# Optimization experiments

Measured on AMD Instinct MI355X. Metric: run time of the kernel, lower is better.

Reference implementation:

```python
import jax, jax.numpy as jnp
import numpy as np

N, E, B = 8192, 131072, 256
F_ATOM, D, H, HD, L, FC, BINS = 92, 256, 8, 32, 6, 512, 256
VMIN, VMAX = 0.0, 8.0


def layer_norm(x, g, b, eps=1e-5):
    mu = jnp.mean(x, axis=-1, keepdims=True)
    var = jnp.var(x, axis=-1, keepdims=True)
    return (x - mu) * jax.lax.rsqrt(var + eps) * g + b


def silu(x):
    return x * jax.nn.sigmoid(x)


def setup_inputs() -> dict:
    key = jax.random.key(0)
    ks = iter(jax.random.split(key, 80))

    def lin(fan_in, shape):
        return jax.random.normal(next(ks), shape, jnp.float32) / np.sqrt(fan_in)

    inp = {
        'x': jax.random.normal(next(ks), (N, F_ATOM), jnp.float32),
        'edge_attr': jax.random.normal(next(ks), (E, 3), jnp.float32) * 2.0,
        'edge_index': jax.random.randint(next(ks), (2, E), 0, N, dtype=jnp.int32),
        'batch': jnp.sort(jax.random.randint(next(ks), (N,), 0, B, dtype=jnp.int32)),
        # atom_embedding: Linear(92,256) -> LN -> SiLU -> Linear(256,256)
        'aw1': lin(F_ATOM, (F_ATOM, D)), 'ab1': jnp.zeros((D,)),
        'ag1': jnp.ones((D,)), 'abt1': jnp.zeros((D,)),
        'aw2': lin(D, (D, D)), 'ab2': jnp.zeros((D,)),
        # rbf MLP: Linear(256,256) LN SiLU Linear LN SiLU Linear
        'rw1': lin(BINS, (BINS, D)), 'rb1': jnp.zeros((D,)),
        'rg1': jnp.ones((D,)), 'rbt1': jnp.zeros((D,)),
        'rw2': lin(D, (D, D)), 'rb2': jnp.zeros((D,)),
        'rg2': jnp.ones((D,)), 'rbt2': jnp.zeros((D,)),
        'rw3': lin(D, (D, D)), 'rb3': jnp.zeros((D,)),
        # L stacked PrdnetConv (edge-conditioned multi-head graph attention)
        'Wq': lin(D, (L, D, D)), 'bq': jnp.zeros((L, D)),
        'Wk': lin(D, (L, D, D)), 'bk': jnp.zeros((L, D)),
        'Wv': lin(D, (L, D, D)), 'bv': jnp.zeros((L, D)),
        'We': lin(D, (L, D, D)), 'be': jnp.zeros((L, D)),
        'Wo': lin(D, (L, D, D)), 'bo': jnp.zeros((L, D)),
        'lng': jnp.ones((L, D)), 'lnb': jnp.zeros((L, D)),
        # FC head: Linear(256,512) then fc_out Linear(512,1)
        'fw1': lin(D, (D, FC)), 'fb1': jnp.zeros((FC,)),
        'fow': lin(FC, (FC, 1)), 'fob': jnp.zeros((1,)),
    }
    return inp


def _forward(x, edge_attr, edge_index, batch, aw1, ab1, ag1, abt1, aw2, ab2,
             rw1, rb1, rg1, rbt1, rw2, rb2, rg2, rbt2, rw3, rb3,
             Wq, bq, Wk, bk, Wv, bv, We, be, Wo, bo, lng, lnb,
             fw1, fb1, fow, fob):
    # atom embedding (dropout = identity at inference)
    node = silu(layer_norm(x @ aw1 + ab1, ag1, abt1)) @ aw2 + ab2  # [N, D]

    # RBF expansion of edge lengths, then edge MLP
    d = jnp.linalg.norm(edge_attr, axis=1)  # [E]
    centers = jnp.linspace(VMIN, VMAX, BINS)
    gamma = 1.0 / (centers[1] - centers[0]) ** 2
    rbf = jnp.exp(-gamma * (d[:, None] - centers[None, :]) ** 2)  # [E, BINS]
    e = silu(layer_norm(rbf @ rw1 + rb1, rg1, rbt1))
    e = silu(layer_norm(e @ rw2 + rb2, rg2, rbt2))
    e = e @ rw3 + rb3  # [E, D]

    src, dst = edge_index[0], edge_index[1]
    inv_sqrt = 1.0 / np.sqrt(HD)
    for l in range(L):
        res = node
        q = (node @ Wq[l] + bq[l]).reshape(N, H, HD)
        k = (node @ Wk[l] + bk[l]).reshape(N, H, HD)
        v = (node @ Wv[l] + bv[l]).reshape(N, H, HD)
        ee = (e @ We[l] + be[l]).reshape(E, H, HD)
        kj = k[src] + ee  # edge-conditioned keys [E, H, HD]
        vj = v[src] + ee  # edge-conditioned values
        score = jnp.sum(q[dst] * kj, axis=-1) * inv_sqrt  # [E, H]
        smax = jax.ops.segment_max(score, dst, num_segments=N)  # [N, H]
        ex = jnp.exp(score - smax[dst])
        den = jax.ops.segment_sum(ex, dst, num_segments=N)
        alpha = ex / (den[dst] + 1e-16)  # neighborhood softmax [E, H]
        msg = jax.ops.segment_sum(alpha[:, :, None] * vj, dst, num_segments=N)
        out = msg.reshape(N, D) @ Wo[l] + bo[l]
        out = layer_norm(out, lng[l], lnb[l])
        node = out + res  # residual

    # scatter-mean graph pooling
    sums = jax.ops.segment_sum(node, batch, num_segments=B)  # [B, D]
    cnt = jax.ops.segment_sum(jnp.ones((N,), node.dtype), batch, num_segments=B)
    feats = sums / jnp.clip(cnt, 1.0)[:, None]

    feats = feats @ fw1 + fb1  # single fc layer: no act (i == len-1 in source)
    return feats @ fow + fob  # [B, 1], identity link


def reference(x, edge_attr, edge_index, batch, aw1, ab1, ag1, abt1, aw2, ab2,
              rw1, rb1, rg1, rbt1, rw2, rb2, rg2, rbt2, rw3, rb3,
              Wq, bq, Wk, bk, Wv, bv, We, be, Wo, bo, lng, lnb,
              fw1, fb1, fow, fob):
    return _forward(x, edge_attr, edge_index, batch, aw1, ab1, ag1, abt1, aw2,
                    ab2, rw1, rb1, rg1, rbt1, rw2, rb2, rg2, rbt2, rw3, rb3,
                    Wq, bq, Wk, bk, Wv, bv, We, be, Wo, bo, lng, lnb,
                    fw1, fb1, fow, fob)
```

## Files before the change

kernel.cpp:

```cpp
#include <hip/hip_runtime.h>
#include <hip/hip_bf16.h>
#include <cstddef>

#define NN    8192
#define EE    131072
#define BB    256
#define F_AT  92
#define DD    256
#define HH    8
#define HDIM  32
#define LL    6
#define FCD   512

typedef __hip_bfloat16 bf16;
typedef __attribute__((ext_vector_type(8))) __bf16 bf16x8;
typedef __attribute__((ext_vector_type(4))) float f32x4;

__device__ __forceinline__ float to_f(float x) { return x; }
__device__ __forceinline__ float to_f(bf16 x) { return __bfloat162float(x); }
__device__ __forceinline__ float bfu(unsigned short u) {
    return __uint_as_float(((unsigned)u) << 16);
}
__device__ __forceinline__ unsigned short bfbits(float x) {
    bf16 h = __float2bfloat16(x);
    return *(unsigned short*)&h;
}
__device__ __forceinline__ void store_v(float* p, float v) { *p = v; }
__device__ __forceinline__ void store_v(bf16* p, float v) { *p = __float2bfloat16(v); }

__device__ __forceinline__ float4 load4(const float* p) { return *(const float4*)p; }
__device__ __forceinline__ float4 load4(const bf16* p) {
    const ushort4 r = *(const ushort4*)p;
    return make_float4(bfu(r.x), bfu(r.y), bfu(r.z), bfu(r.w));
}

__device__ __forceinline__ void store_f4(float* p, const float4& f) {
    *(float4*)p = f;
}
__device__ __forceinline__ void store_f4(bf16* p, const float4& f) {
    ushort4 u = {bfbits(f.x), bfbits(f.y), bfbits(f.z), bfbits(f.w)};
    *(ushort4*)p = u;
}

__device__ __forceinline__ bf16x8 ld8(const bf16* p) { return *(const bf16x8*)p; }
__device__ __forceinline__ bf16x8 ld8(const float* p) {
    const float4 f0 = *(const float4*)p;
    const float4 f1 = *(const float4*)(p + 4);
    bf16x8 r;
    r[0] = (__bf16)f0.x; r[1] = (__bf16)f0.y; r[2] = (__bf16)f0.z; r[3] = (__bf16)f0.w;
    r[4] = (__bf16)f1.x; r[5] = (__bf16)f1.y; r[6] = (__bf16)f1.z; r[7] = (__bf16)f1.w;
    return r;
}

__device__ __forceinline__ void async_copy16(const void* g, void* l) {
    __builtin_amdgcn_global_load_lds(
        (const __attribute__((address_space(1))) unsigned int*)g,
        (__attribute__((address_space(3))) unsigned int*)l, 16, 0, 0);
}

__global__ __launch_bounds__(256) void transpose_weights(
    const float* __restrict__ rw1, const float* __restrict__ rw2,
    const float* __restrict__ rw3, const float* __restrict__ aw2,
    const float* __restrict__ Wq, const float* __restrict__ Wk,
    const float* __restrict__ Wv, const float* __restrict__ We,
    const float* __restrict__ Wo, __bf16* __restrict__ out)
{
    __shared__ float tile[64][65];
    const int midx = blockIdx.y;
    const float* src;
    int fam = 0, s = 0;
    if (midx == 0) src = rw1;
    else if (midx == 1) src = rw2;
    else if (midx == 2) src = rw3;
    else if (midx == 3) src = aw2;
    else {
        fam = (midx - 4) / 5; s = (midx - 4) % 5;
        const float* bases[5] = {Wq, Wk, Wv, We, Wo};
        src = bases[s] + (size_t)fam * 65536;
    }
    const bool isqkv = (midx >= 4) && (s < 3);
    __bf16* dstb = isqkv ? (out + (size_t)(4 + 5 * fam) * 65536)
                         : (out + (size_t)midx * 65536);
    const int k0 = (blockIdx.x >> 2) * 64;
    const int n0 = (blockIdx.x & 3) * 64;
    const int c = threadIdx.x & 63;
    const int r0 = threadIdx.x >> 6;
#pragma unroll
    for (int p = 0; p < 16; ++p) {
        const int r = r0 + p * 4;
        tile[r][c] = src[(size_t)(k0 + r) * 256 + n0 + c];
    }
    __syncthreads();
#pragma unroll
    for (int p = 0; p < 16; ++p) {
        const int n = r0 + p * 4;
        const int gr = n0 + n;
        int row = gr;
        if (isqkv) {
            if (s == 1)      row = 256 + ((gr >> 2) << 3) + (gr & 3);
            else if (s == 2) row = 256 + ((gr >> 2) << 3) + 4 + (gr & 3);
        }
        dstb[(size_t)row * 256 + k0 + c] = (__bf16)tile[c][n];
    }
}

__global__ __launch_bounds__(256) void pack_qkv_bias(
    const float* __restrict__ bq, const float* __restrict__ bk,
    const float* __restrict__ bv, float* __restrict__ out)
{
    const int i = blockIdx.x * 256 + threadIdx.x;
    if (i >= LL * 768) return;
    const int l = i / 768, r = i % 768;
    float val; int pos;
    if (r < 256)      { val = bq[l * 256 + r];        pos = r; }
    else if (r < 512) { const int c = r - 256; val = bk[l * 256 + c];
                        pos = 256 + ((c >> 2) << 3) + (c & 3); }
    else              { const int c = r - 512; val = bv[l * 256 + c];
                        pos = 256 + ((c >> 2) << 3) + 4 + (c & 3); }
    out[l * 768 + pos] = val;
}

__global__ __launch_bounds__(256) void combine_w3e(
    const float* __restrict__ rw3, const float* __restrict__ We,
    __bf16* __restrict__ Wt_out)
{
    __shared__ float As[16][65];
    __shared__ float Ws[16][65];
    const int l = blockIdx.z;
    const float* W = We + (size_t)l * 65536;
    __bf16* dst = Wt_out + (size_t)l * 65536;
    const int m0 = blockIdx.x * 64;
    const int n0 = blockIdx.y * 64;
    const int tid = threadIdx.x;
    const int tx = tid & 15, ty = tid >> 4;
    float acc[4][4] = {};

    for (int k0 = 0; k0 < 256; k0 += 16) {
        {
            const int ar = tid >> 2;
            const int ac = (tid & 3) * 4;
#pragma unroll
            for (int j = 0; j < 4; ++j)
                As[ac + j][ar] = rw3[(size_t)(m0 + ar) * 256 + k0 + ac + j];
        }
        {
            const int wr = tid >> 4;
            const int wc = (tid & 15) * 4;
#pragma unroll
            for (int j = 0; j < 4; ++j)
                Ws[wr][wc + j] = W[(size_t)(k0 + wr) * 256 + n0 + wc + j];
        }
        __syncthreads();
#pragma unroll
        for (int kk = 0; kk < 16; ++kk) {
            float a[4], b[4];
#pragma unroll
            for (int i = 0; i < 4; ++i) a[i] = As[kk][ty * 4 + i];
#pragma unroll
            for (int j = 0; j < 4; ++j) b[j] = Ws[kk][tx * 4 + j];
#pragma unroll
            for (int i = 0; i < 4; ++i)
#pragma unroll
                for (int j = 0; j < 4; ++j) acc[i][j] += a[i] * b[j];
        }
        __syncthreads();
    }
#pragma unroll
    for (int i = 0; i < 4; ++i) {
        const int gk = m0 + ty * 4 + i;
#pragma unroll
        for (int j = 0; j < 4; ++j) {
            const int gn = n0 + tx * 4 + j;
            dst[(size_t)gn * 256 + gk] = (__bf16)acc[i][j];
        }
    }
}

__global__ __launch_bounds__(256) void combine_bias(
    const float* __restrict__ rb3, const float* __restrict__ We,
    const float* __restrict__ be, float* __restrict__ out)
{
    const int l = blockIdx.x;
    const int n = threadIdx.x;
    const float* W = We + (size_t)l * 65536;
    float s = be[l * 256 + n];
    for (int m = 0; m < 256; ++m) s += rb3[m] * W[m * 256 + n];
    out[l * 256 + n] = s;
}

__global__ __launch_bounds__(256) void mfma_gemm_ln(
    const bf16* __restrict__ A, const __bf16* __restrict__ Wt,
    const float* __restrict__ bias, const float* __restrict__ g,
    const float* __restrict__ b, bf16* __restrict__ C, int do_silu)
{
    __shared__ __align__(16) __bf16 As[64 * 64];
    __shared__ __align__(16) __bf16 Bs[256 * 64];
    const int tid = threadIdx.x;
    const int m0 = blockIdx.x * 64;
    const int wave = tid >> 6, lane = tid & 63;
    const int lm = lane & 15, lq = lane >> 4;
    const int lrow = lane >> 3;
    const int lcolsw = ((lane & 7) ^ lrow) * 8;

    f32x4 acc[16] = {};

    for (int k0 = 0; k0 < 256; k0 += 64) {
#pragma unroll
        for (int p = 0; p < 2; ++p) {
            const int rbase = wave * 16 + p * 8;
            async_copy16(A + (size_t)(m0 + rbase + lrow) * 256 + k0 + lcolsw,
                         As + rbase * 64);
        }
#pragma unroll
        for (int p = 0; p < 8; ++p) {
            const int rbase = wave * 64 + p * 8;
            async_copy16(Wt + (size_t)(rbase + lrow) * 256 + k0 + lcolsw,
                         Bs + rbase * 64);
        }
        __syncthreads();
#pragma unroll
        for (int ks = 0; ks < 2; ++ks) {
            const int sw = ((ks * 4 + lq) ^ (lm & 7)) * 8;
            const bf16x8 a = *(const bf16x8*)(As + (wave * 16 + lm) * 64 + sw);
#pragma unroll
            for (int j = 0; j < 16; ++j) {
                const bf16x8 bf = *(const bf16x8*)(Bs + (j * 16 + lm) * 64 + sw);
                acc[j] = __builtin_amdgcn_mfma_f32_16x16x32_bf16(a, bf, acc[j], 0, 0, 0);
            }
        }
        __syncthreads();
    }

    float gg[16], bb[16];
#pragma unroll
    for (int j = 0; j < 16; ++j) {
        const float bv = bias[j * 16 + lm];
        gg[j] = g[j * 16 + lm];
        bb[j] = b[j * 16 + lm];
#pragma unroll
        for (int r = 0; r < 4; ++r) acc[j][r] += bv;
    }

#pragma unroll
    for (int r = 0; r < 4; ++r) {
        float s = 0.f, q = 0.f;
#pragma unroll
        for (int j = 0; j < 16; ++j) { const float v = acc[j][r]; s += v; q += v * v; }
#pragma unroll
        for (int msk = 1; msk < 16; msk <<= 1) {
            s += __shfl_xor(s, msk);
            q += __shfl_xor(q, msk);
        }
        const float mean = s * (1.f / 256.f);
        const float var = q * (1.f / 256.f) - mean * mean;
        const float rs = rsqrtf(var + 1e-5f);
        __bf16* erow = Bs + (wave * 16 + lq * 4 + r) * 256;
#pragma unroll
        for (int j = 0; j < 16; ++j) {
            float v = (acc[j][r] - mean) * rs * gg[j] + bb[j];
            if (do_silu) v = v / (1.f + __expf(-v));
            erow[j * 16 + lm] = (__bf16)v;
        }
    }
    __syncthreads();
    {
        __bf16* cbase = (__bf16*)C + (size_t)m0 * 256;
#pragma unroll
        for (int p = 0; p < 8; ++p) {
            const int ofs = (tid + p * 256) * 8;
            *(bf16x8*)(cbase + ofs) = *(const bf16x8*)(Bs + ofs);
        }
    }
}

__global__ __launch_bounds__(256) void mfma_gemm_ln_rbf(
    const float* __restrict__ dcsr, const __bf16* __restrict__ Wt,
    const float* __restrict__ bias, const float* __restrict__ g,
    const float* __restrict__ b, bf16* __restrict__ C)
{
    __shared__ __align__(16) __bf16 As[64 * 64];
    __shared__ __align__(16) __bf16 Bs[256 * 64];
    const int tid = threadIdx.x;
    const int m0 = blockIdx.x * 64;
    const int wave = tid >> 6, lane = tid & 63;
    const int lm = lane & 15, lq = lane >> 4;
    const int lrow = lane >> 3;
    const int lcolsw = ((lane & 7) ^ lrow) * 8;

    const float step = 8.0f / 255.0f;
    const float gamma = 1.0f / (step * step);

    float dv[2];
#pragma unroll
    for (int p = 0; p < 2; ++p)
        dv[p] = dcsr[m0 + wave * 16 + p * 8 + lrow];

    f32x4 acc[16] = {};

    for (int k0 = 0; k0 < 256; k0 += 64) {
#pragma unroll
        for (int p = 0; p < 2; ++p) {
            const int r = wave * 16 + p * 8 + lrow;
            __bf16* dst8 = As + r * 64 + (lane & 7) * 8;
            const int cbase = k0 + lcolsw;
#pragma unroll
            for (int j = 0; j < 8; ++j) {
                const float t = dv[p] - (float)(cbase + j) * step;
                dst8[j] = (__bf16)__expf(-gamma * t * t);
            }
        }
#pragma unroll
        for (int p = 0; p < 8; ++p) {
            const int rbase = wave * 64 + p * 8;
            async_copy16(Wt + (size_t)(rbase + lrow) * 256 + k0 + lcolsw,
                         Bs + rbase * 64);
        }
        __syncthreads();
#pragma unroll
        for (int ks = 0; ks < 2; ++ks) {
            const int sw = ((ks * 4 + lq) ^ (lm & 7)) * 8;
            const bf16x8 a = *(const bf16x8*)(As + (wave * 16 + lm) * 64 + sw);
#pragma unroll
            for (int j = 0; j < 16; ++j) {
                const bf16x8 bf = *(const bf16x8*)(Bs + (j * 16 + lm) * 64 + sw);
                acc[j] = __builtin_amdgcn_mfma_f32_16x16x32_bf16(a, bf, acc[j], 0, 0, 0);
            }
        }
        __syncthreads();
    }

    float gg[16], bb[16];
#pragma unroll
    for (int j = 0; j < 16; ++j) {
        const float bv = bias[j * 16 + lm];
        gg[j] = g[j * 16 + lm];
        bb[j] = b[j * 16 + lm];
#pragma unroll
        for (int r = 0; r < 4; ++r) acc[j][r] += bv;
    }

#pragma unroll
    for (int r = 0; r < 4; ++r) {
        float s = 0.f, q = 0.f;
#pragma unroll
        for (int j = 0; j < 16; ++j) { const float v = acc[j][r]; s += v; q += v * v; }
#pragma unroll
        for (int msk = 1; msk < 16; msk <<= 1) {
            s += __shfl_xor(s, msk);
            q += __shfl_xor(q, msk);
        }
        const float mean = s * (1.f / 256.f);
        const float var = q * (1.f / 256.f) - mean * mean;
        const float rs = rsqrtf(var + 1e-5f);
        __bf16* erow = Bs + (wave * 16 + lq * 4 + r) * 256;
#pragma unroll
        for (int j = 0; j < 16; ++j) {
            float v = (acc[j][r] - mean) * rs * gg[j] + bb[j];
            v = v / (1.f + __expf(-v));
            erow[j * 16 + lm] = (__bf16)v;
        }
    }
    __syncthreads();
    {
        __bf16* cbase = (__bf16*)C + (size_t)m0 * 256;
#pragma unroll
        for (int p = 0; p < 8; ++p) {
            const int ofs = (tid + p * 256) * 8;
            *(bf16x8*)(cbase + ofs) = *(const bf16x8*)(Bs + ofs);
        }
    }
}

__global__ __launch_bounds__(256) void mfma_gemm_ln_res(
    const float* __restrict__ A, const __bf16* __restrict__ Wt,
    const float* __restrict__ bias, const float* __restrict__ g,
    const float* __restrict__ b, float* __restrict__ node)
{
    __shared__ __align__(16) __bf16 As[64 * 72];
    __shared__ __align__(16) __bf16 Bs[256 * 64];
    const int tid = threadIdx.x;
    const int m0 = blockIdx.x * 64;
    const int wave = tid >> 6, lane = tid & 63;
    const int lm = lane & 15, lq = lane >> 4;
    const int lrow = lane >> 3;
    const int lcolsw = ((lane & 7) ^ lrow) * 8;

    f32x4 acc[16] = {};
    const int srow = tid >> 3;
    const int scol = (tid & 7) * 8;

    for (int k0 = 0; k0 < 256; k0 += 64) {
#pragma unroll
        for (int p = 0; p < 2; ++p) {
            const int r = srow + 32 * p;
            *(bf16x8*)(As + r * 72 + scol) = ld8(A + (size_t)(m0 + r) * 256 + k0 + scol);
        }
#pragma unroll
        for (int p = 0; p < 8; ++p) {
            const int rbase = wave * 64 + p * 8;
            async_copy16(Wt + (size_t)(rbase + lrow) * 256 + k0 + lcolsw,
                         Bs + rbase * 64);
        }
        __syncthreads();
#pragma unroll
        for (int ks = 0; ks < 2; ++ks) {
            const int sw = ((ks * 4 + lq) ^ (lm & 7)) * 8;
            const bf16x8 a = *(const bf16x8*)(As + (wave * 16 + lm) * 72 + ks * 32 + lq * 8);
#pragma unroll
            for (int j = 0; j < 16; ++j) {
                const bf16x8 bf = *(const bf16x8*)(Bs + (j * 16 + lm) * 64 + sw);
                acc[j] = __builtin_amdgcn_mfma_f32_16x16x32_bf16(a, bf, acc[j], 0, 0, 0);
            }
        }
        __syncthreads();
    }

    float gg[16], bb[16];
#pragma unroll
    for (int j = 0; j < 16; ++j) {
        const float bv = bias[j * 16 + lm];
        gg[j] = g[j * 16 + lm];
        bb[j] = b[j * 16 + lm];
#pragma unroll
        for (int r = 0; r < 4; ++r) acc[j][r] += bv;
    }

#pragma unroll
    for (int r = 0; r < 4; ++r) {
        float s = 0.f, q = 0.f;
#pragma unroll
        for (int j = 0; j < 16; ++j) { const float v = acc[j][r]; s += v; q += v * v; }
#pragma unroll
        for (int msk = 1; msk < 16; msk <<= 1) {
            s += __shfl_xor(s, msk);
            q += __shfl_xor(q, msk);
        }
        const float mean = s * (1.f / 256.f);
        const float var = q * (1.f / 256.f) - mean * mean;
        const float rs = rsqrtf(var + 1e-5f);
        float* crow = node + (size_t)(m0 + wave * 16 + lq * 4 + r) * 256;
#pragma unroll
        for (int j = 0; j < 16; ++j) {
            const float v = (acc[j][r] - mean) * rs * gg[j] + bb[j];
            crow[j * 16 + lm] += v;
        }
    }
}

__global__ __launch_bounds__(256) void mfma_gemm_ee(
    const bf16* __restrict__ A, const __bf16* __restrict__ Wt,
    const float* __restrict__ bias, bf16* __restrict__ C,
    int M, int Nn, int K)
{
    __shared__ __align__(16) __bf16 smem[128 * 128];
    __bf16* As = smem;
    __bf16* Bs = smem + 128 * 64;
    const int tid = threadIdx.x;

    const int nt_n = Nn >> 7;
    const int xcd = blockIdx.x & 7;
    const int local = blockIdx.x >> 3;
    const int per_xcd = (M >> 7) >> 3;
    const int m0 = (xcd * per_xcd + local / nt_n) * 128;
    const int n0 = (local % nt_n) * 128;

    const int wave = tid >> 6, lane = tid & 63;
    const int wm = (wave & 1) * 64, wn = (wave >> 1) * 64;
    const int lm = lane & 15, lq = lane >> 4;
    const int lrow = lane >> 3;
    const int lcolsw = ((lane & 7) ^ lrow) * 8;

    f32x4 acc[4][4] = {};

    for (int k0 = 0; k0 < K; k0 += 64) {
#pragma unroll
        for (int p = 0; p < 4; ++p) {
            const int rbase = wave * 32 + p * 8;
            async_copy16(A  + (size_t)(m0 + rbase + lrow) * K + k0 + lcolsw,
                         As + rbase * 64);
            async_copy16(Wt + (size_t)(n0 + rbase + lrow) * K + k0 + lcolsw,
                         Bs + rbase * 64);
        }
        __syncthreads();
#pragma unroll
        for (int ks = 0; ks < 2; ++ks) {
            const int sw = ((ks * 4 + lq) ^ (lm & 7)) * 8;
            bf16x8 a[4], b[4];
#pragma unroll
            for (int i = 0; i < 4; ++i) {
                a[i] = *(const bf16x8*)(As + (wm + i * 16 + lm) * 64 + sw);
                b[i] = *(const bf16x8*)(Bs + (wn + i * 16 + lm) * 64 + sw);
            }
#pragma unroll
            for (int i = 0; i < 4; ++i)
#pragma unroll
                for (int j = 0; j < 4; ++j)
                    acc[i][j] = __builtin_amdgcn_mfma_f32_16x16x32_bf16(
                        a[i], b[j], acc[i][j], 0, 0, 0);
        }
        __syncthreads();
    }

#pragma unroll
    for (int i = 0; i < 4; ++i) {
        const int rl = wm + i * 16 + lq * 4;
#pragma unroll
        for (int j = 0; j < 4; ++j) {
            const int cl = wn + j * 16 + lm;
            const float bb = bias ? bias[n0 + cl] : 0.f;
#pragma unroll
            for (int r = 0; r < 4; ++r) {
                const int row = rl + r;
                smem[row * 128 + (cl ^ ((row & 7) << 3))] =
                    (__bf16)(acc[i][j][r] + bb);
            }
        }
    }
    __syncthreads();
#pragma unroll
    for (int p = 0; p < 8; ++p) {
        const int ch = tid + p * 256;
        const int row = ch >> 4;
        const int gcol = ch & 15;
        const int sg = gcol ^ (row & 7);
        *(bf16x8*)((__bf16*)C + (size_t)(m0 + row) * Nn + n0 + gcol * 8) =
            *(const bf16x8*)(smem + row * 128 + sg * 8);
    }
}

template <typename CT>
__global__ __launch_bounds__(256) void mfma_gemm64(
    const float* __restrict__ A, const __bf16* __restrict__ Wt,
    const float* __restrict__ bias, CT* __restrict__ C,
    int M, int Nn, int K)
{
    __shared__ __align__(16) __bf16 As[64 * 72];
    __shared__ __align__(16) __bf16 Bs[128 * 72];
    const int tid = threadIdx.x;
    const int m0 = blockIdx.x * 64;
    const int n0 = blockIdx.y * 128;
    const int wave = tid >> 6, lane = tid & 63;
    const int wm = (wave & 1) * 32, wn = (wave >> 1) * 64;
    const int lm = lane & 15, lq = lane >> 4;

    f32x4 acc[2][4] = {};

    const int srow = tid >> 3;
    const int scol = (tid & 7) * 8;

    for (int k0 = 0; k0 < K; k0 += 64) {
#pragma unroll
        for (int p = 0; p < 2; ++p) {
            const int r = srow + 32 * p;
            *(bf16x8*)(As + r * 72 + scol) =
                ld8(A + (size_t)(m0 + r) * K + k0 + scol);
        }
#pragma unroll
        for (int p = 0; p < 4; ++p) {
            const int r = srow + 32 * p;
            *(bf16x8*)(Bs + r * 72 + scol) =
                *(const bf16x8*)(Wt + (size_t)(n0 + r) * K + k0 + scol);
        }
        __syncthreads();
#pragma unroll
        for (int ks = 0; ks < 2; ++ks) {
            bf16x8 a[2], b[4];
#pragma unroll
            for (int i = 0; i < 2; ++i)
                a[i] = *(const bf16x8*)(As + (wm + i * 16 + lm) * 72 + ks * 32 + lq * 8);
#pragma unroll
            for (int j = 0; j < 4; ++j)
                b[j] = *(const bf16x8*)(Bs + (wn + j * 16 + lm) * 72 + ks * 32 + lq * 8);
#pragma unroll
            for (int i = 0; i < 2; ++i)
#pragma unroll
                for (int j = 0; j < 4; ++j)
                    acc[i][j] = __builtin_amdgcn_mfma_f32_16x16x32_bf16(
                        a[i], b[j], acc[i][j], 0, 0, 0);
        }
        __syncthreads();
    }

#pragma unroll
    for (int i = 0; i < 2; ++i) {
        const int gm = m0 + wm + i * 16 + lq * 4;
#pragma unroll
        for (int j = 0; j < 4; ++j) {
            const int gn = n0 + wn + j * 16 + lm;
            const float bv = bias ? bias[gn] : 0.f;
#pragma unroll
            for (int r = 0; r < 4; ++r)
                store_v(&C[(size_t)(gm + r) * Nn + gn], acc[i][j][r] + bv);
        }
    }
}

template <typename AT, typename CT>
__global__ __launch_bounds__(256) void gemm_bias(
    const AT* __restrict__ A, const float* __restrict__ W,
    const float* __restrict__ bias, CT* __restrict__ C,
    int M, int Nn, int K, const float* __restrict__ cntdiv)
{
    __shared__ float As[16][65];
    __shared__ float Ws[16][65];
    const int m0 = blockIdx.x * 64;
    const int n0 = blockIdx.y * 64;
    const int tid = threadIdx.x;
    const int tx = tid & 15, ty = tid >> 4;
    float acc[4][4] = {};

    for (int k0 = 0; k0 < K; k0 += 16) {
        {
            const int ar = tid >> 2;
            const int ac = (tid & 3) * 4;
            const int gm = m0 + ar;
            float inv = 1.f;
            if (cntdiv && gm < M) {
                float cc = cntdiv[gm];
                if (cc < 1.f) cc = 1.f;
                inv = 1.f / cc;
            }
#pragma unroll
            for (int j = 0; j < 4; ++j) {
                const int gk = k0 + ac + j;
                float v = 0.f;
                if (gm < M && gk < K) v = to_f(A[(size_t)gm * K + gk]) * inv;
                As[ac + j][ar] = v;
            }
        }
        {
            const int wr = tid >> 4;
            const int wc = (tid & 15) * 4;
            const int gk = k0 + wr;
#pragma unroll
            for (int j = 0; j < 4; ++j) {
                float v = 0.f;
                if (gk < K) v = W[(size_t)gk * Nn + n0 + wc + j];
                Ws[wr][wc + j] = v;
            }
        }
        __syncthreads();
#pragma unroll
        for (int kk = 0; kk < 16; ++kk) {
            float a[4], b[4];
#pragma unroll
            for (int i = 0; i < 4; ++i) a[i] = As[kk][ty * 4 + i];
#pragma unroll
            for (int j = 0; j < 4; ++j) b[j] = Ws[kk][tx * 4 + j];
#pragma unroll
            for (int i = 0; i < 4; ++i)
#pragma unroll
                for (int j = 0; j < 4; ++j) acc[i][j] += a[i] * b[j];
        }
        __syncthreads();
    }
#pragma unroll
    for (int i = 0; i < 4; ++i) {
        const int gm = m0 + ty * 4 + i;
        if (gm >= M) continue;
#pragma unroll
        for (int j = 0; j < 4; ++j) {
            const int gn = n0 + tx * 4 + j;
            float v = acc[i][j];
            if (bias) v += bias[gn];
            store_v(&C[(size_t)gm * Nn + gn], v);
        }
    }
}

template <typename XT, typename YT>
__global__ __launch_bounds__(256) void ln_act_kernel(
    const XT* __restrict__ X, YT* __restrict__ Y,
    const float* __restrict__ g, const float* __restrict__ b,
    const float* __restrict__ resid, int rows, int do_silu)
{
    const int wave = threadIdx.x >> 6;
    const int lane = threadIdx.x & 63;
    const int r = blockIdx.x * 4 + wave;
    if (r >= rows) return;
    const float4 x = load4(X + (size_t)r * DD + lane * 4);
    float s = x.x + x.y + x.z + x.w;
    float q = x.x * x.x + x.y * x.y + x.z * x.z + x.w * x.w;
    for (int off = 32; off; off >>= 1) {
        s += __shfl_down(s, off);
        q += __shfl_down(q, off);
    }
    s = __shfl(s, 0);
    q = __shfl(q, 0);
    const float mean = s * (1.f / 256.f);
    const float var = q * (1.f / 256.f) - mean * mean;
    const float rs = rsqrtf(var + 1e-5f);
    const int c = lane * 4;
    float xs[4] = {x.x, x.y, x.z, x.w};
    float out[4];
#pragma unroll
    for (int i = 0; i < 4; ++i) {
        float v = (xs[i] - mean) * rs * g[c + i] + b[c + i];
        if (do_silu) v = v / (1.f + __expf(-v));
        out[i] = v;
    }
    if (resid) {
        const float4 rv = load4(resid + (size_t)r * DD + c);
        out[0] += rv.x; out[1] += rv.y; out[2] += rv.z; out[3] += rv.w;
    }
    store_f4(Y + (size_t)r * DD + c, make_float4(out[0], out[1], out[2], out[3]));
}

__global__ __launch_bounds__(256) void deg_kernel(
    const int* __restrict__ dst, int* __restrict__ deg)
{
    const int e = blockIdx.x * 256 + threadIdx.x;
    if (e < EE) atomicAdd(&deg[dst[e]], 1);
}

__global__ __launch_bounds__(256) void csr_scan(
    const int* __restrict__ deg, int* __restrict__ rowptr)
{
    __shared__ int part[256];
    const int t = threadIdx.x;
    int local[32];
    int s = 0;
#pragma unroll
    for (int i = 0; i < 32; ++i) { local[i] = deg[t * 32 + i]; s += local[i]; }
    part[t] = s;
    __syncthreads();
    if (t == 0) {
        int run = 0;
        for (int i = 0; i < 256; ++i) { const int v = part[i]; part[i] = run; run += v; }
    }
    __syncthreads();
    int run = part[t];
#pragma unroll
    for (int i = 0; i < 32; ++i) { rowptr[t * 32 + i] = run; run += local[i]; }
    if (t == 255) rowptr[NN] = run;
}

__global__ __launch_bounds__(256) void fill_kernel(
    const int* __restrict__ src, const int* __restrict__ dst,
    const float* __restrict__ ea, const int* __restrict__ rowptr,
    int* __restrict__ fill, int* __restrict__ eid,
    int* __restrict__ srcc, float* __restrict__ dcsr)
{
    const int e = blockIdx.x * 256 + threadIdx.x;
    if (e >= EE) return;
    const int d = dst[e];
    const int pos = atomicAdd(&fill[d], 1);
    const int q = rowptr[d] + pos;
    eid[q] = e;
    srcc[q] = src[e];
    const float ax = ea[e * 3 + 0];
    const float ay = ea[e * 3 + 1];
    const float az = ea[e * 3 + 2];
    dcsr[q] = sqrtf(ax * ax + ay * ay + az * az);
}

__global__ __launch_bounds__(256) void attn_kernel(
    const bf16* __restrict__ qkv, const bf16* __restrict__ ee, int estride,
    const int* __restrict__ rowptr, const int* __restrict__ srcc,
    float* __restrict__ msg)
{
    const int n = blockIdx.x;
    const int tid = threadIdx.x;
    const int wave = tid >> 6, lane = tid & 63;
    const int e0 = rowptr[n];
    const int deg = rowptr[n + 1] - e0;

    if (deg == 0) {
        msg[(size_t)n * DD + tid] = 0.f;
        return;
    }

    __shared__ float wm[4][HH];
    __shared__ float wl[4][HH];
    __shared__ float wacc[4][DD];

    const float4 qreg = load4(qkv + (size_t)n * 768 + lane * 4);

    float m = -3.402823466e38f, l = 0.f;
    float4 acc = {0.f, 0.f, 0.f, 0.f};

    int j = wave;
    bf16x8 kvp = {};
    float4 ev = {0.f, 0.f, 0.f, 0.f};
    if (j < deg) {
        const int e = e0 + j;
        const bf16* srow = qkv + (size_t)srcc[e] * 768;
        kvp = ld8(srow + 256 + lane * 8);
        ev = load4(ee + (size_t)e * estride + lane * 4);
    }
    while (j < deg) {
        const int jn = j + 4;
        bf16x8 kvp2 = {};
        float4 ev2 = {0.f, 0.f, 0.f, 0.f};
        if (jn < deg) {
            const int e2 = e0 + jn;
            const bf16* srow2 = qkv + (size_t)srcc[e2] * 768;
            kvp2 = ld8(srow2 + 256 + lane * 8);
            ev2 = load4(ee + (size_t)e2 * estride + lane * 4);
        }
        const float kx = (float)kvp[0], ky = (float)kvp[1];
        const float kz = (float)kvp[2], kw = (float)kvp[3];
        const float vx = (float)kvp[4], vy = (float)kvp[5];
        const float vz = (float)kvp[6], vw = (float)kvp[7];
        float p = qreg.x * (kx + ev.x) + qreg.y * (ky + ev.y) +
                  qreg.z * (kz + ev.z) + qreg.w * (kw + ev.w);
        p += __shfl_down(p, 4);
        p += __shfl_down(p, 2);
        p += __shfl_down(p, 1);
        const float s = __shfl(p, lane & 56) * 0.17677669529663687f;
        const float mnew = fmaxf(m, s);
        const float scale = __expf(m - mnew);
        const float pe = __expf(s - mnew);
        l = l * scale + pe;
        acc.x = acc.x * scale + pe * (vx + ev.x);
        acc.y = acc.y * scale + pe * (vy + ev.y);
        acc.z = acc.z * scale + pe * (vz + ev.z);
        acc.w = acc.w * scale + pe * (vw + ev.w);
        m = mnew;
        kvp = kvp2; ev = ev2;
        j = jn;
    }

    if ((lane & 7) == 0) { wm[wave][lane >> 3] = m; wl[wave][lane >> 3] = l; }
    *(float4*)(&wacc[wave][lane * 4]) = acc;
    __syncthreads();

    {
        const int c = tid, h = tid >> 5;
        float M = wm[0][h];
#pragma unroll
        for (int i = 1; i < 4; ++i) M = fmaxf(M, wm[i][h]);
        float L = 0.f, num = 0.f;
#pragma unroll
        for (int i = 0; i < 4; ++i) {
            const float sc = __expf(wm[i][h] - M);
            L += wl[i][h] * sc;
            num += wacc[i][c] * sc;
        }
        msg[(size_t)n * DD + c] = num / (L + 1e-16f);
    }
}

__global__ __launch_bounds__(256) void zero_kernel(float* __restrict__ p, int n)
{
    const int i = blockIdx.x * 256 + threadIdx.x;
    if (i < n) p[i] = 0.f;
}

__global__ __launch_bounds__(256) void pool_kernel(
    const float* __restrict__ node, const int* __restrict__ batch,
    float* __restrict__ sums, float* __restrict__ cnt)
{
    const int n = blockIdx.x;
    const int c = threadIdx.x;
    const int b = batch[n];
    atomicAdd(&sums[b * DD + c], node[(size_t)n * DD + c]);
    if (c == 0) atomicAdd(&cnt[b], 1.0f);
}

__global__ __launch_bounds__(64) void final_kernel(
    const float* __restrict__ fc, const float* __restrict__ fow,
    const float* __restrict__ fob, float* __restrict__ out)
{
    const int b = blockIdx.x;
    const int lane = threadIdx.x;
    float s = 0.f;
#pragma unroll
    for (int i = lane; i < FCD; i += 64) s += fc[(size_t)b * FCD + i] * fow[i];
    for (int off = 32; off; off >>= 1) s += __shfl_down(s, off);
    if (lane == 0) out[b] = s + fob[0];
}

extern "C" void kernel_launch(void* const* d_in, const int* in_sizes, int n_in,
                              void* d_out, int out_size, void* d_ws,
                              size_t ws_size, hipStream_t stream)
{
    const float* x         = (const float*)d_in[0];
    const float* edge_attr = (const float*)d_in[1];
    const int*   eidx      = (const int*)d_in[2];
    const int*   batch     = (const int*)d_in[3];
    const float* aw1 = (const float*)d_in[4];
    const float* ab1 = (const float*)d_in[5];
    const float* ag1 = (const float*)d_in[6];
    const float* abt1 = (const float*)d_in[7];
    const float* aw2 = (const float*)d_in[8];
    const float* ab2 = (const float*)d_in[9];
    const float* rw1 = (const float*)d_in[10];
    const float* rb1 = (const float*)d_in[11];
    const float* rg1 = (const float*)d_in[12];
    const float* rbt1 = (const float*)d_in[13];
    const float* rw2 = (const float*)d_in[14];
    const float* rb2 = (const float*)d_in[15];
    const float* rg2 = (const float*)d_in[16];
    const float* rbt2 = (const float*)d_in[17];
    const float* rw3 = (const float*)d_in[18];
    const float* rb3 = (const float*)d_in[19];
    const float* Wq = (const float*)d_in[20];
    const float* bq = (const float*)d_in[21];
    const float* Wk = (const float*)d_in[22];
    const float* bk = (const float*)d_in[23];
    const float* Wv = (const float*)d_in[24];
    const float* bv = (const float*)d_in[25];
    const float* We_ = (const float*)d_in[26];
    const float* be_ = (const float*)d_in[27];
    const float* Wo = (const float*)d_in[28];
    const float* bo = (const float*)d_in[29];
    const float* lng = (const float*)d_in[30];
    const float* lnb = (const float*)d_in[31];
    const float* fw1 = (const float*)d_in[32];
    const float* fb1 = (const float*)d_in[33];
    const float* fow = (const float*)d_in[34];
    const float* fob = (const float*)d_in[35];

    const int* src = eidx;
    const int* dst = eidx + EE;

    char* w = (char*)d_ws;
    size_t off = 0;
    auto alloc = [&](size_t bytes) -> void* {
        void* p = w + off;
        off += (bytes + 255) & ~(size_t)255;
        return p;
    };
    bf16* t_buf = (bf16*)alloc((size_t)EE * DD * 2);
    float* node = (float*)alloc((size_t)NN * DD * 4);
    bf16*  qkv  = (bf16*)alloc((size_t)NN * 768 * 2);
    float* msg  = (float*)alloc((size_t)NN * DD * 4);
    float* outb = (float*)alloc((size_t)NN * DD * 4);
    int* deg    = (int*)alloc((size_t)NN * 4);
    int* fillc  = (int*)alloc((size_t)NN * 4);
    int* rowptr = (int*)alloc((size_t)(NN + 1) * 4);
    int* eid    = (int*)alloc((size_t)EE * 4);
    int* srcc   = (int*)alloc((size_t)EE * 4);
    float* dcsr = (float*)alloc((size_t)EE * 4);
    float* sums  = (float*)alloc((size_t)BB * DD * 4);
    float* cnt   = (float*)alloc((size_t)BB * 4);
    float* fc    = (float*)alloc((size_t)BB * FCD * 4);
    __bf16* Wt  = (__bf16*)alloc((size_t)40 * 65536 * 2);
    float* qkvb = (float*)alloc((size_t)LL * 768 * 4);
    float* be_c = (float*)alloc((size_t)LL * 256 * 4);

    const size_t avail = (off <= ws_size) ? ws_size - off : 0;
    int G = 1;
    if      (avail >= (size_t)EE * (6 * DD) * 2 + 256) G = 6;
    else if (avail >= (size_t)EE * (3 * DD) * 2 + 256) G = 3;
    else if (avail >= (size_t)EE * (2 * DD) * 2 + 256) G = 2;
    bf16* e_slab = (bf16*)alloc((size_t)EE * (G * DD) * 2);
    (void)n_in; (void)in_sizes; (void)out_size;

    const dim3 blk(256);
    auto WT = [&](int i) -> const __bf16* { return Wt + (size_t)i * 65536; };

    hipLaunchKernelGGL(transpose_weights, dim3(16, 34), blk, 0, stream,
                       rw1, rw2, rw3, aw2, Wq, Wk, Wv, We_, Wo, Wt);
    hipLaunchKernelGGL(combine_w3e, dim3(4, 4, LL), blk, 0, stream, rw3, We_, Wt + (size_t)34 * 65536);
    hipLaunchKernelGGL(combine_bias, dim3(LL), blk, 0, stream, rb3, We_, be_, be_c);
    hipLaunchKernelGGL(pack_qkv_bias, dim3((LL * 768 + 255) / 256), blk, 0, stream, bq, bk, bv, qkvb);
    hipLaunchKernelGGL(zero_kernel, dim3((2 * NN + 255) / 256), blk, 0, stream, (float*)deg, 2 * NN);
    hipLaunchKernelGGL(deg_kernel, dim3(EE / 256), blk, 0, stream, dst, deg);
    hipLaunchKernelGGL(csr_scan, dim3(1), blk, 0, stream, deg, rowptr);
    hipLaunchKernelGGL(fill_kernel, dim3(EE / 256), blk, 0, stream, src, dst, edge_attr, rowptr, fillc, eid, srcc, dcsr);

    hipLaunchKernelGGL(mfma_gemm_ln_rbf, dim3(EE / 64), blk, 0, stream, dcsr, WT(0), rb1, rg1, rbt1, e_slab);
    hipLaunchKernelGGL(mfma_gemm_ln, dim3(EE / 64), blk, 0, stream, e_slab, WT(1), rb2, rg2, rbt2, t_buf, 1);

    {
        dim3 gn64(NN / 64, DD / 64);
        hipLaunchKernelGGL((gemm_bias<float, float>), gn64, blk, 0, stream, x, aw1, ab1, outb, NN, DD, F_AT, (const float*)nullptr);
        hipLaunchKernelGGL((ln_act_kernel<float, float>), dim3(NN / 4), blk, 0, stream, outb, outb, ag1, abt1, (const float*)nullptr, NN, 1);
        hipLaunchKernelGGL((mfma_gemm64<float>), dim3(NN / 64, DD / 128), blk, 0, stream, outb, WT(3), ab2, node, NN, DD, DD);
    }

    for (int l = 0; l < LL; ++l) {
        const size_t bo_ = (size_t)l * DD;
        hipLaunchKernelGGL((mfma_gemm64<bf16>), dim3(NN / 64, 768 / 128), blk, 0, stream,
                           node, WT(4 + 5 * l), qkvb + (size_t)l * 768, qkv, NN, 768, DD);
        if (l % G == 0) {
            const int nblocks = (EE / 128) * ((G * DD) / 128);
            hipLaunchKernelGGL(mfma_gemm_ee, dim3(nblocks), blk, 0, stream,
                               t_buf, WT(34 + l), be_c + (size_t)l * 256, e_slab, EE, G * DD, DD);
        }
        const bf16* ee_l = e_slab + (size_t)(l % G) * DD;
        hipLaunchKernelGGL(attn_kernel, dim3(NN), blk, 0, stream, qkv, ee_l, G * DD, rowptr, srcc, msg);
        hipLaunchKernelGGL(mfma_gemm_ln_res, dim3(NN / 64), blk, 0, stream,
                           msg, WT(8 + 5 * l), bo + bo_, lng + bo_, lnb + bo_, node);
    }

    const int PZ = BB * DD + BB;
    hipLaunchKernelGGL(zero_kernel, dim3((PZ + 255) / 256), blk, 0, stream, sums, PZ);
    hipLaunchKernelGGL(pool_kernel, dim3(NN), blk, 0, stream, node, batch, sums, cnt);
    {
        dim3 gf(BB / 64, FCD / 64);
        hipLaunchKernelGGL((gemm_bias<float, float>), gf, blk, 0, stream, sums, fw1, fb1, fc, BB, FCD, DD, cnt);
    }
    hipLaunchKernelGGL(final_kernel, dim3(BB), dim3(64), 0, stream, fc, fow, fob, (float*)d_out);
}
```

Before: 927.5 us.

## Fuse edge-projection GEMM with QKV GEMM launch and store attention messages in bf16

Merges the edge-feature GEMM and the node QKV GEMM into one launch, with block index deciding which GEMM a block runs. This removes a kernel launch and lets the small QKV GEMM fill the tail of the large edge GEMM. The attention output buffer also becomes bf16 instead of fp32, halving its write and read traffic into the output-projection GEMM, at some cost in precision. The mfma_gemm_ln_res kernel now takes bf16 input, which depends on its load helper handling bf16.

```diff
diff --git a/kernel.cpp b/kernel.cpp
--- a/kernel.cpp
+++ b/kernel.cpp
@@ -372,7 +372,7 @@
 }
 
 __global__ __launch_bounds__(256) void mfma_gemm_ln_res(
-    const float* __restrict__ A, const __bf16* __restrict__ Wt,
+    const bf16* __restrict__ A, const __bf16* __restrict__ Wt,
     const float* __restrict__ bias, const float* __restrict__ g,
     const float* __restrict__ b, float* __restrict__ node)
 {
@@ -447,84 +447,145 @@
     }
 }
 
-__global__ __launch_bounds__(256) void mfma_gemm_ee(
-    const bf16* __restrict__ A, const __bf16* __restrict__ Wt,
-    const float* __restrict__ bias, bf16* __restrict__ C,
-    int M, int Nn, int K)
+__global__ __launch_bounds__(256) void ee_qkv_fused(
+    const bf16* __restrict__ A, const __bf16* __restrict__ Wte,
+    const float* __restrict__ biase, bf16* __restrict__ Ce,
+    int M, int Nn, int K, int nblk_ee,
+    const float* __restrict__ nodeA, const __bf16* __restrict__ Wtq,
+    const float* __restrict__ biasq, bf16* __restrict__ Cq)
 {
     __shared__ __align__(16) __bf16 smem[128 * 128];
-    __bf16* As = smem;
-    __bf16* Bs = smem + 128 * 64;
     const int tid = threadIdx.x;
-
-    const int nt_n = Nn >> 7;
-    const int xcd = blockIdx.x & 7;
-    const int local = blockIdx.x >> 3;
-    const int per_xcd = (M >> 7) >> 3;
-    const int m0 = (xcd * per_xcd + local / nt_n) * 128;
-    const int n0 = (local % nt_n) * 128;
-
     const int wave = tid >> 6, lane = tid & 63;
-    const int wm = (wave & 1) * 64, wn = (wave >> 1) * 64;
     const int lm = lane & 15, lq = lane >> 4;
-    const int lrow = lane >> 3;
-    const int lcolsw = ((lane & 7) ^ lrow) * 8;
-
-    f32x4 acc[4][4] = {};
-
-    for (int k0 = 0; k0 < K; k0 += 64) {
-#pragma unroll
-        for (int p = 0; p < 4; ++p) {
-            const int rbase = wave * 32 + p * 8;
-            async_copy16(A  + (size_t)(m0 + rbase + lrow) * K + k0 + lcolsw,
-                         As + rbase * 64);
-            async_copy16(Wt + (size_t)(n0 + rbase + lrow) * K + k0 + lcolsw,
-                         Bs + rbase * 64);
-        }
-        __syncthreads();
-#pragma unroll
-        for (int ks = 0; ks < 2; ++ks) {
-            const int sw = ((ks * 4 + lq) ^ (lm & 7)) * 8;
-            bf16x8 a[4], b[4];
-#pragma unroll
-            for (int i = 0; i < 4; ++i) {
-                a[i] = *(const bf16x8*)(As + (wm + i * 16 + lm) * 64 + sw);
-                b[i] = *(const bf16x8*)(Bs + (wn + i * 16 + lm) * 64 + sw);
-            }
-#pragma unroll
-            for (int i = 0; i < 4; ++i)
+
+    if ((int)blockIdx.x < nblk_ee) {
+        __bf16* As = smem;
+        __bf16* Bs = smem + 128 * 64;
+        const int nt_n = Nn >> 7;
+        const int xcd = blockIdx.x & 7;
+        const int local = blockIdx.x >> 3;
+        const int per_xcd = (M >> 7) >> 3;
+        const int m0 = (xcd * per_xcd + local / nt_n) * 128;
+        const int n0 = (local % nt_n) * 128;
+
+        const int wm = (wave & 1) * 64, wn = (wave >> 1) * 64;
+        const int lrow = lane >> 3;
+        const int lcolsw = ((lane & 7) ^ lrow) * 8;
+
+        f32x4 acc[4][4] = {};
+
+        for (int k0 = 0; k0 < K; k0 += 64) {
+#pragma unroll
+            for (int p = 0; p < 4; ++p) {
+                const int rbase = wave * 32 + p * 8;
+                async_copy16(A   + (size_t)(m0 + rbase + lrow) * K + k0 + lcolsw,
+                             As + rbase * 64);
+                async_copy16(Wte + (size_t)(n0 + rbase + lrow) * K + k0 + lcolsw,
+                             Bs + rbase * 64);
+            }
+            __syncthreads();
+#pragma unroll
+            for (int ks = 0; ks < 2; ++ks) {
+                const int sw = ((ks * 4 + lq) ^ (lm & 7)) * 8;
+                bf16x8 a[4], b[4];
+#pragma unroll
+                for (int i = 0; i < 4; ++i) {
+                    a[i] = *(const bf16x8*)(As + (wm + i * 16 + lm) * 64 + sw);
+                    b[i] = *(const bf16x8*)(Bs + (wn + i * 16 + lm) * 64 + sw);
+                }
+#pragma unroll
+                for (int i = 0; i < 4; ++i)
+#pragma unroll
+                    for (int j = 0; j < 4; ++j)
+                        acc[i][j] = __builtin_amdgcn_mfma_f32_16x16x32_bf16(
+                            a[i], b[j], acc[i][j], 0, 0, 0);
+            }
+            __syncthreads();
+        }
+
+#pragma unroll
+        for (int i = 0; i < 4; ++i) {
+            const int rl = wm + i * 16 + lq * 4;
+#pragma unroll
+            for (int j = 0; j < 4; ++j) {
+                const int cl = wn + j * 16 + lm;
+                const float bb = biase ? biase[n0 + cl] : 0.f;
+#pragma unroll
+                for (int r = 0; r < 4; ++r) {
+                    const int row = rl + r;
+                    smem[row * 128 + (cl ^ ((row & 7) << 3))] =
+                        (__bf16)(acc[i][j][r] + bb);
+                }
+            }
+        }
+        __syncthreads();
+#pragma unroll
+        for (int p = 0; p < 8; ++p) {
+            const int ch = tid + p * 256;
+            const int row = ch >> 4;
+            const int gcol = ch & 15;
+            const int sg = gcol ^ (row & 7);
+            *(bf16x8*)((__bf16*)Ce + (size_t)(m0 + row) * Nn + n0 + gcol * 8) =
+                *(const bf16x8*)(smem + row * 128 + sg * 8);
+        }
+    } else {
+        const int bq = blockIdx.x - nblk_ee;
+        const int m0 = (bq % (NN / 64)) * 64;
+        const int n0 = (bq / (NN / 64)) * 128;
+        __bf16* As = smem;
+        __bf16* Bs = smem + 64 * 72;
+
+        const int wm = (wave & 1) * 32, wn = (wave >> 1) * 64;
+        f32x4 acc[2][4] = {};
+        const int srow = tid >> 3;
+        const int scol = (tid & 7) * 8;
+
+        for (int k0 = 0; k0 < 256; k0 += 64) {
+#pragma unroll
+            for (int p = 0; p < 2; ++p) {
+                const int r = srow + 32 * p;
+                *(bf16x8*)(As + r * 72 + scol) =
+                    ld8(nodeA + (size_t)(m0 + r) * 256 + k0 + scol);
+            }
+#pragma unroll
+            for (int p = 0; p < 4; ++p) {
+                const int r = srow + 32 * p;
+                *(bf16x8*)(Bs + r * 72 + scol) =
+                    *(const bf16x8*)(Wtq + (size_t)(n0 + r) * 256 + k0 + scol);
+            }
+            __syncthreads();
+#pragma unroll
+            for (int ks = 0; ks < 2; ++ks) {
+                bf16x8 a[2], b[4];
+#pragma unroll
+                for (int i = 0; i < 2; ++i)
+                    a[i] = *(const bf16x8*)(As + (wm + i * 16 + lm) * 72 + ks * 32 + lq * 8);
 #pragma unroll
                 for (int j = 0; j < 4; ++j)
-                    acc[i][j] = __builtin_amdgcn_mfma_f32_16x16x32_bf16(
-                        a[i], b[j], acc[i][j], 0, 0, 0);
-        }
-        __syncthreads();
-    }
-
-#pragma unroll
-    for (int i = 0; i < 4; ++i) {
-        const int rl = wm + i * 16 + lq * 4;
-#pragma unroll
-        for (int j = 0; j < 4; ++j) {
-            const int cl = wn + j * 16 + lm;
-            const float bb = bias ? bias[n0 + cl] : 0.f;
-#pragma unroll
-            for (int r = 0; r < 4; ++r) {
-                const int row = rl + r;
-                smem[row * 128 + (cl ^ ((row & 7) << 3))] =
-                    (__bf16)(acc[i][j][r] + bb);
-            }
-        }
-    }
-    __syncthreads();
-#pragma unroll
-    for (int p = 0; p < 8; ++p) {
-        const int ch = tid + p * 256;
-        const int row = ch >> 4;
-        const int gcol = ch & 15;
-        const int sg = gcol ^ (row & 7);
-        *(bf16x8*)((__bf16*)C + (size_t)(m0 + row) * Nn + n0 + gcol * 8) =
-            *(const bf16x8*)(smem + row * 128 + sg * 8);
+                    b[j] = *(const bf16x8*)(Bs + (wn + j * 16 + lm) * 72 + ks * 32 + lq * 8);
+#pragma unroll
+                for (int i = 0; i < 2; ++i)
+#pragma unroll
+                    for (int j = 0; j < 4; ++j)
+                        acc[i][j] = __builtin_amdgcn_mfma_f32_16x16x32_bf16(
+                            a[i], b[j], acc[i][j], 0, 0, 0);
+            }
+            __syncthreads();
+        }
+
+#pragma unroll
+        for (int i = 0; i < 2; ++i) {
+            const int gm = m0 + wm + i * 16 + lq * 4;
+#pragma unroll
+            for (int j = 0; j < 4; ++j) {
+                const int gn = n0 + wn + j * 16 + lm;
+                const float bv = biasq[gn];
+#pragma unroll
+                for (int r = 0; r < 4; ++r)
+                    store_v(&Cq[(size_t)(gm + r) * 768 + gn], acc[i][j][r] + bv);
+            }
+        }
     }
 }
 
@@ -757,7 +818,7 @@
 __global__ __launch_bounds__(256) void attn_kernel(
     const bf16* __restrict__ qkv, const bf16* __restrict__ ee, int estride,
     const int* __restrict__ rowptr, const int* __restrict__ srcc,
-    float* __restrict__ msg)
+    bf16* __restrict__ msg)
 {
     const int n = blockIdx.x;
     const int tid = threadIdx.x;
@@ -766,7 +827,7 @@
     const int deg = rowptr[n + 1] - e0;
 
     if (deg == 0) {
-        msg[(size_t)n * DD + tid] = 0.f;
+        store_v(&msg[(size_t)n * DD + tid], 0.f);
         return;
     }
 
@@ -837,7 +898,7 @@
             L += wl[i][h] * sc;
             num += wacc[i][c] * sc;
         }
-        msg[(size_t)n * DD + c] = num / (L + 1e-16f);
+        store_v(&msg[(size_t)n * DD + c], num / (L + 1e-16f));
     }
 }
 
@@ -925,7 +986,7 @@
     bf16* t_buf = (bf16*)alloc((size_t)EE * DD * 2);
     float* node = (float*)alloc((size_t)NN * DD * 4);
     bf16*  qkv  = (bf16*)alloc((size_t)NN * 768 * 2);
-    float* msg  = (float*)alloc((size_t)NN * DD * 4);
+    bf16*  msg  = (bf16*)alloc((size_t)NN * DD * 2);
     float* outb = (float*)alloc((size_t)NN * DD * 4);
     int* deg    = (int*)alloc((size_t)NN * 4);
     int* fillc  = (int*)alloc((size_t)NN * 4);
@@ -971,14 +1032,16 @@
         hipLaunchKernelGGL((mfma_gemm64<float>), dim3(NN / 64, DD / 128), blk, 0, stream, outb, WT(3), ab2, node, NN, DD, DD);
     }
 
+    const int nblk_ee = (EE / 128) * ((G * DD) / 128);
     for (int l = 0; l < LL; ++l) {
         const size_t bo_ = (size_t)l * DD;
-        hipLaunchKernelGGL((mfma_gemm64<bf16>), dim3(NN / 64, 768 / 128), blk, 0, stream,
-                           node, WT(4 + 5 * l), qkvb + (size_t)l * 768, qkv, NN, 768, DD);
         if (l % G == 0) {
-            const int nblocks = (EE / 128) * ((G * DD) / 128);
-            hipLaunchKernelGGL(mfma_gemm_ee, dim3(nblocks), blk, 0, stream,
-                               t_buf, WT(34 + l), be_c + (size_t)l * 256, e_slab, EE, G * DD, DD);
+            hipLaunchKernelGGL(ee_qkv_fused, dim3(nblk_ee + (NN / 64) * (768 / 128)), blk, 0, stream,
+                               t_buf, WT(34 + l), be_c + (size_t)l * 256, e_slab, EE, G * DD, DD, nblk_ee,
+                               node, WT(4 + 5 * l), qkvb + (size_t)l * 768, qkv);
+        } else {
+            hipLaunchKernelGGL((mfma_gemm64<bf16>), dim3(NN / 64, 768 / 128), blk, 0, stream,
+                               node, WT(4 + 5 * l), qkvb + (size_t)l * 768, qkv, NN, 768, DD);
         }
         const bf16* ee_l = e_slab + (size_t)(l % G) * DD;
         hipLaunchKernelGGL(attn_kernel, dim3(NN), blk, 0, stream, qkv, ee_l, G * DD, rowptr, srcc, msg);
```

Result: no change. 923.1 us (-0.5%).
